# Kernel optimization log

Hardware: AMD Instinct MI355X
Metric: run time of the kernel (lower is better)

Reference implementation:

```python
import jax, jax.numpy as jnp
import numpy as np


def sobel_kernels_3d(dtype=jnp.float32):
    # Standard 3D Sobel: derivative [-1,0,1] along one axis, smoothing [1,2,1]
    # along the other two. Returns shape (3, 1, 3, 3, 3) in OIDHW layout.
    s = jnp.array([1.0, 2.0, 1.0], dtype=dtype)
    d = jnp.array([-1.0, 0.0, 1.0], dtype=dtype)
    kd = jnp.einsum('i,j,k->ijk', d, s, s)  # d/dD
    kh = jnp.einsum('i,j,k->ijk', s, d, s)  # d/dH
    kw = jnp.einsum('i,j,k->ijk', s, s, d)  # d/dW
    return jnp.stack([kd, kh, kw], axis=0)[:, None]  # (3,1,3,3,3)


def _grad3d(x, kernels):
    # x: (B, C, D, H, W) -> flatten (B*C, 1, D, H, W), conv with padding=1.
    B, C, D, H, W = x.shape
    x_ = x.reshape(B * C, 1, D, H, W)
    return jax.lax.conv_general_dilated(
        x_, kernels.astype(x.dtype),
        window_strides=(1, 1, 1),
        padding=((1, 1), (1, 1), (1, 1)),
        dimension_numbers=('NCDHW', 'OIDHW', 'NCDHW'),
    )  # (B*C, 3, D, H, W)


def setup_inputs() -> dict:
    key = jax.random.key(0)
    k1, k2 = jax.random.split(key)
    shape = (4, 4, 64, 128, 128)
    pred = jax.random.normal(k1, shape, dtype=jnp.float32)
    target = jax.random.normal(k2, shape, dtype=jnp.float32)
    return {"pred": pred, "target": target}


def reference(pred, target):
    kernels = sobel_kernels_3d(pred.dtype)
    grad_pred = _grad3d(pred, kernels)
    grad_target = _grad3d(target, kernels)
    # loss_type == 'l1'
    return jnp.mean(jnp.abs(grad_pred - grad_target))
```

## Files before the change

### kernel.cpp

```cpp
#include <hip/hip_runtime.h>

#define NB 16
#define DD 64
#define HH 128
#define WW 128
#define HW (HH * WW)

constexpr int CD = 2;
constexpr int TH = 8;
constexpr int LZ = CD + 2;
constexpr int LY = TH + 2;
constexpr int PL = LY * WW;
constexpr int NPOS = LZ * LY * (WW / 4);
constexpr int SLOTS = NPOS / 256;
constexpr int NT = 8;
constexpr float INV_COUNT = 1.0f / 50331648.0f;

__global__ void zero_out_kernel(float* out) {
    if (threadIdx.x == 0 && blockIdx.x == 0) out[0] = 0.0f;
}

__global__ __launch_bounds__(256) void sobel_l1_kernel(
    const float* __restrict__ pred,
    const float* __restrict__ target,
    float* __restrict__ out)
{
    __shared__ float t[2][LZ * PL];

    const int tid = threadIdx.x;
    int b = blockIdx.x;
    const int bh = b & 15; b >>= 4;
    const int qt = b & 3;  b >>= 2;
    const int bn = b;

    const int h0 = bh * TH;
    const int dbase = qt * (NT * CD);
    const size_t nbase = (size_t)bn * (size_t)(DD * HW);

    int  soff[SLOTS];
    int  sz[SLOTS];
    bool sokh[SLOTS];
#pragma unroll
    for (int k = 0; k < SLOTS; ++k) {
        const int i  = k * 256 + tid;
        const int q4 = i & 31;
        const int ry = i >> 5;
        const int z  = ry / LY;
        const int y  = ry - z * LY;
        const int gh = h0 - 1 + y;
        sokh[k] = (unsigned)gh < HH;
        soff[k] = min(max(gh, 0), HH - 1) * WW + 4 * q4;
        sz[k]   = z;
    }

    float4 sp[SLOTS], sq[SLOTS];

    auto load_tile = [&](int tau) {
        const int d0 = dbase + tau * CD;
#pragma unroll
        for (int k = 0; k < SLOTS; ++k) {
            const int gd  = d0 - 1 + sz[k];
            const int gdc = min(max(gd, 0), DD - 1);
            const size_t idx = nbase + (size_t)gdc * HW + soff[k];
            sp[k] = *(const float4*)(pred + idx);
            sq[k] = *(const float4*)(target + idx);
        }
    };

    auto store_tile = [&](int tau, float* B) {
        const int d0 = dbase + tau * CD;
#pragma unroll
        for (int k = 0; k < SLOTS; ++k) {
            const int gd = d0 - 1 + sz[k];
            const float m = (sokh[k] && (unsigned)gd < DD) ? 1.0f : 0.0f;
            const int i = k * 256 + tid;
            const float4 v = float4{(sp[k].x - sq[k].x) * m,
                                    (sp[k].y - sq[k].y) * m,
                                    (sp[k].z - sq[k].z) * m,
                                    (sp[k].w - sq[k].w) * m};
            *(float4*)&B[4 * i] = v;
        }
    };

    const int tc = tid & 31;
    const int lh = tid >> 5;

    auto compute_tile = [&](const float* B, float& acc) {
        auto plane_l = [&](int z, float4& A_, float4& Bh_, float4& Bw_) {
            float4 rs[3], rdw[3];
#pragma unroll
            for (int r = 0; r < 3; ++r) {
                const float4 v = *(const float4*)&B[z * PL + (lh + r) * WW + 4 * tc];
                float lm = __shfl_up(v.w, 1, 32);
                float rp = __shfl_down(v.x, 1, 32);
                if (tc == 0)  lm = 0.f;
                if (tc == 31) rp = 0.f;
                rs[r]  = float4{lm  + 2.f * v.x + v.y,
                                v.x + 2.f * v.y + v.z,
                                v.y + 2.f * v.z + v.w,
                                v.z + 2.f * v.w + rp};
                rdw[r] = float4{v.y - lm, v.z - v.x, v.w - v.y, rp - v.z};
            }
            A_  = float4{rs[0].x + 2.f * rs[1].x + rs[2].x,
                         rs[0].y + 2.f * rs[1].y + rs[2].y,
                         rs[0].z + 2.f * rs[1].z + rs[2].z,
                         rs[0].w + 2.f * rs[1].w + rs[2].w};
            Bh_ = float4{rs[2].x - rs[0].x, rs[2].y - rs[0].y,
                         rs[2].z - rs[0].z, rs[2].w - rs[0].w};
            Bw_ = float4{rdw[0].x + 2.f * rdw[1].x + rdw[2].x,
                         rdw[0].y + 2.f * rdw[1].y + rdw[2].y,
                         rdw[0].z + 2.f * rdw[1].z + rdw[2].z,
                         rdw[0].w + 2.f * rdw[1].w + rdw[2].w};
        };

        float4 rA[3], rBh[3], rBw[3];
        plane_l(0, rA[0], rBh[0], rBw[0]);
        plane_l(1, rA[1], rBh[1], rBw[1]);
#pragma unroll
        for (int ld = 0; ld < CD; ++ld) {
            const int s0 = ld % 3, s1 = (ld + 1) % 3, s2 = (ld + 2) % 3;
            plane_l(ld + 2, rA[s2], rBh[s2], rBw[s2]);
            const float4 a0 = rA[s0],  a2 = rA[s2];
            const float4 b0 = rBh[s0], b1 = rBh[s1], b2 = rBh[s2];
            const float4 c0 = rBw[s0], c1 = rBw[s1], c2 = rBw[s2];
            acc += fabsf(a2.x - a0.x) + fabsf(a2.y - a0.y)
                 + fabsf(a2.z - a0.z) + fabsf(a2.w - a0.w);
            acc += fabsf(b0.x + 2.f * b1.x + b2.x) + fabsf(b0.y + 2.f * b1.y + b2.y)
                 + fabsf(b0.z + 2.f * b1.z + b2.z) + fabsf(b0.w + 2.f * b1.w + b2.w);
            acc += fabsf(c0.x + 2.f * c1.x + c2.x) + fabsf(c0.y + 2.f * c1.y + c2.y)
                 + fabsf(c0.z + 2.f * c1.z + c2.z) + fabsf(c0.w + 2.f * c1.w + c2.w);
        }
    };

    float acc = 0.0f;
    load_tile(0);
    store_tile(0, t[0]);
    __syncthreads();
    for (int tau = 0; tau < NT; ++tau) {
        if (tau + 1 < NT) load_tile(tau + 1);
        compute_tile(t[tau & 1], acc);
        if (tau + 1 < NT) store_tile(tau + 1, t[(tau + 1) & 1]);
        __syncthreads();
    }

#pragma unroll
    for (int off = 32; off > 0; off >>= 1)
        acc += __shfl_down(acc, off, 64);
    if ((tid & 63) == 0) t[0][tid >> 6] = acc;
    __syncthreads();
    if (tid == 0) {
        const float s = t[0][0] + t[0][1] + t[0][2] + t[0][3];
        atomicAdd(out, s * INV_COUNT);
    }
}

extern "C" void kernel_launch(void* const* d_in, const int* in_sizes, int n_in,
                              void* d_out, int out_size, void* d_ws, size_t ws_size,
                              hipStream_t stream) {
    const float* pred   = (const float*)d_in[0];
    const float* target = (const float*)d_in[1];
    float* out = (float*)d_out;

    zero_out_kernel<<<1, 64, 0, stream>>>(out);

    const int nblocks = NB * 4 * (HH / TH);
    sobel_l1_kernel<<<nblocks, 256, 0, stream>>>(pred, target, out);
}
```

Baseline: 156.0 us.

## Give each wavefront a private LDS slab and drop block-wide barriers

Each of the four wavefronts now stages its own 4-row slab (2 output rows plus halo) of the pred−target difference in shared memory. Because a wave only reads what it wrote, the per-iteration __syncthreads in the depth loop is removed, so waves progress independently. In exchange, halo rows are loaded per wave instead of once per block, which raises global/L2 load traffic and per-thread load slots (5→8), and LDS use grows. Correctness relies on wave-level ordering of LDS writes and reads without an explicit barrier.

```diff
diff --git a/kernel.cpp b/kernel.cpp
--- a/kernel.cpp
+++ b/kernel.cpp
@@ -6,14 +6,13 @@
 #define WW 128
 #define HW (HH * WW)
 
-constexpr int CD = 2;
-constexpr int TH = 8;
-constexpr int LZ = CD + 2;
-constexpr int LY = TH + 2;
-constexpr int PL = LY * WW;
-constexpr int NPOS = LZ * LY * (WW / 4);
-constexpr int SLOTS = NPOS / 256;
-constexpr int NT = 8;
+constexpr int CD  = 2;
+constexpr int TH  = 8;
+constexpr int LZ  = CD + 2;
+constexpr int LYW = 4;
+constexpr int NT  = 8;
+constexpr int SLAB = LZ * LYW * WW;
+constexpr int SLOTS = 8;
 constexpr float INV_COUNT = 1.0f / 50331648.0f;
 
 __global__ void zero_out_kernel(float* out) {
@@ -25,7 +24,8 @@
     const float* __restrict__ target,
     float* __restrict__ out)
 {
-    __shared__ float t[2][LZ * PL];
+    __shared__ float t[2][4 * SLAB];
+    __shared__ float wsum[4];
 
     const int tid = threadIdx.x;
     int b = blockIdx.x;
@@ -33,7 +33,12 @@
     const int qt = b & 3;  b >>= 2;
     const int bn = b;
 
-    const int h0 = bh * TH;
+    const int wh  = tid >> 6;
+    const int lane = tid & 63;
+    const int tc  = lane & 31;
+    const int lr  = lane >> 5;
+
+    const int hw0 = bh * TH + wh * 2;
     const int dbase = qt * (NT * CD);
     const size_t nbase = (size_t)bn * (size_t)(DD * HW);
 
@@ -41,16 +46,15 @@
     int  sz[SLOTS];
     bool sokh[SLOTS];
 #pragma unroll
-    for (int k = 0; k < SLOTS; ++k) {
-        const int i  = k * 256 + tid;
-        const int q4 = i & 31;
-        const int ry = i >> 5;
-        const int z  = ry / LY;
-        const int y  = ry - z * LY;
-        const int gh = h0 - 1 + y;
-        sokh[k] = (unsigned)gh < HH;
-        soff[k] = min(max(gh, 0), HH - 1) * WW + 4 * q4;
-        sz[k]   = z;
+    for (int j = 0; j < SLOTS; ++j) {
+        const int s  = 64 * j + lane;
+        const int q4 = s & 31;
+        const int row = s >> 5;
+        const int y  = row & 3;
+        sz[j] = row >> 2;
+        const int gh = hw0 - 1 + y;
+        sokh[j] = (unsigned)gh < HH;
+        soff[j] = min(max(gh, 0), HH - 1) * WW + 4 * q4;
     }
 
     float4 sp[SLOTS], sq[SLOTS];
@@ -58,39 +62,36 @@
     auto load_tile = [&](int tau) {
         const int d0 = dbase + tau * CD;
 #pragma unroll
-        for (int k = 0; k < SLOTS; ++k) {
-            const int gd  = d0 - 1 + sz[k];
+        for (int j = 0; j < SLOTS; ++j) {
+            const int gd  = d0 - 1 + sz[j];
             const int gdc = min(max(gd, 0), DD - 1);
-            const size_t idx = nbase + (size_t)gdc * HW + soff[k];
-            sp[k] = *(const float4*)(pred + idx);
-            sq[k] = *(const float4*)(target + idx);
+            const size_t idx = nbase + (size_t)gdc * HW + soff[j];
+            sp[j] = *(const float4*)(pred + idx);
+            sq[j] = *(const float4*)(target + idx);
         }
     };
 
     auto store_tile = [&](int tau, float* B) {
         const int d0 = dbase + tau * CD;
 #pragma unroll
-        for (int k = 0; k < SLOTS; ++k) {
-            const int gd = d0 - 1 + sz[k];
-            const float m = (sokh[k] && (unsigned)gd < DD) ? 1.0f : 0.0f;
-            const int i = k * 256 + tid;
-            const float4 v = float4{(sp[k].x - sq[k].x) * m,
-                                    (sp[k].y - sq[k].y) * m,
-                                    (sp[k].z - sq[k].z) * m,
-                                    (sp[k].w - sq[k].w) * m};
-            *(float4*)&B[4 * i] = v;
+        for (int j = 0; j < SLOTS; ++j) {
+            const int gd = d0 - 1 + sz[j];
+            const float m = (sokh[j] && (unsigned)gd < DD) ? 1.0f : 0.0f;
+            const int s = 64 * j + lane;
+            const float4 v = float4{(sp[j].x - sq[j].x) * m,
+                                    (sp[j].y - sq[j].y) * m,
+                                    (sp[j].z - sq[j].z) * m,
+                                    (sp[j].w - sq[j].w) * m};
+            *(float4*)&B[4 * s] = v;
         }
     };
-
-    const int tc = tid & 31;
-    const int lh = tid >> 5;
 
     auto compute_tile = [&](const float* B, float& acc) {
         auto plane_l = [&](int z, float4& A_, float4& Bh_, float4& Bw_) {
             float4 rs[3], rdw[3];
 #pragma unroll
             for (int r = 0; r < 3; ++r) {
-                const float4 v = *(const float4*)&B[z * PL + (lh + r) * WW + 4 * tc];
+                const float4 v = *(const float4*)&B[(z * LYW + lr + r) * WW + 4 * tc];
                 float lm = __shfl_up(v.w, 1, 32);
                 float rp = __shfl_down(v.x, 1, 32);
                 if (tc == 0)  lm = 0.f;
@@ -132,24 +133,25 @@
         }
     };
 
+    float* slab0 = &t[0][wh * SLAB];
+    float* slab1 = &t[1][wh * SLAB];
     float acc = 0.0f;
+
     load_tile(0);
-    store_tile(0, t[0]);
-    __syncthreads();
+    store_tile(0, slab0);
     for (int tau = 0; tau < NT; ++tau) {
         if (tau + 1 < NT) load_tile(tau + 1);
-        compute_tile(t[tau & 1], acc);
-        if (tau + 1 < NT) store_tile(tau + 1, t[(tau + 1) & 1]);
-        __syncthreads();
+        compute_tile((tau & 1) ? slab1 : slab0, acc);
+        if (tau + 1 < NT) store_tile(tau + 1, (tau & 1) ? slab0 : slab1);
     }
 
 #pragma unroll
     for (int off = 32; off > 0; off >>= 1)
         acc += __shfl_down(acc, off, 64);
-    if ((tid & 63) == 0) t[0][tid >> 6] = acc;
+    if ((tid & 63) == 0) wsum[wh] = acc;
     __syncthreads();
     if (tid == 0) {
-        const float s = t[0][0] + t[0][1] + t[0][2] + t[0][3];
+        const float s = wsum[0] + wsum[1] + wsum[2] + wsum[3];
         atomicAdd(out, s * INV_COUNT);
     }
 }
```

New measurement: 157.2 us. No clear change (+0.8%).
